# Kernel optimization log

Hardware: AMD Instinct MI355X
Metric: run time of the kernel (lower is better)

## Reference

```python
import jax, jax.numpy as jnp
import numpy as np

MARGIN = 0.5  # hardcoded in the torch __init__ regardless of the margin arg
P_IDS, K_PER_ID, K_PER_MOD = 32, 8, 4
B, C = P_IDS * K_PER_ID, 1024


def setup_inputs() -> dict:
    key = jax.random.key(0)
    inputs = jax.random.normal(key, (B, C), dtype=jnp.float32)
    # Standard cross-modal ReID sampler: P identities, K instances each,
    # first K/2 from modality 0, last K/2 from modality 1. This guarantees the
    # boolean-mask reshape in the original code is well-formed (M per row).
    targets = jnp.repeat(jnp.arange(P_IDS, dtype=jnp.int32), K_PER_ID)
    subs = jnp.tile(jnp.repeat(jnp.arange(2, dtype=jnp.int32), K_PER_MOD), P_IDS)
    return {"inputs": inputs, "targets": targets, "subs": subs, "m_count": K_PER_MOD}


def _loss(inputs, targets, subs, m_count):
    b, c = inputs.shape
    # Mask construction uses detached inputs in the original (clone().detach()).
    xs = jax.lax.stop_gradient(inputs)
    diff = jnp.abs(xs[:, None, :] - xs[None, :, :])                     # (B,B,C)
    identity_mask = targets[:, None] == targets[None, :]                # (B,B)
    modality_mask = subs[:, None] == subs[None, :]                      # (B,B)
    combined = identity_mask & modality_mask                            # (B,B)

    # diff[combined].reshape(B, M, C): every row has exactly m_count trues;
    # stable argsort recovers the selected column indices in ascending order,
    # matching torch's row-major boolean-mask gather.
    order = jnp.argsort(jnp.where(combined, 0, 1), axis=1)              # stable
    idx = order[:, :m_count]                                            # (B,M)
    modality_diff = jnp.take_along_axis(diff, idx[:, :, None], axis=1)  # (B,M,C)

    mean_md = modality_diff.mean(-1, keepdims=True)                     # (B,M,1)
    m_counts = (modality_diff < mean_md * MARGIN).sum(1)                # (B,C) int
    # mdm[i,j,c] = m_counts[i,c] * m_counts[j,c]  (detached float mask)
    mdm = (m_counts[:, None, :] * m_counts[None, :, :]).astype(inputs.dtype)  # (B,B,C)

    mean_d = diff.mean(-1, keepdims=True)                               # (B,B,1)
    idm = (diff < mean_d * MARGIN).astype(inputs.dtype)                 # (B,B,C)

    # Gradient-carrying pairwise differences (vectorized form of the B-loop).
    d = inputs[:, None, :] - inputs[None, :, :]                         # (B,B,C)
    mod_dist = jnp.sqrt(jnp.maximum(((d * mdm) ** 2).sum(-1), 1e-12))   # (B,B)
    id_dist = jnp.sqrt(jnp.maximum(((d * idm) ** 2).sum(-1), 1e-12))    # (B,B)
    id_dist = jnp.where(identity_mask, jnp.inf, id_dist)                # drop same-id

    per_row = jnp.maximum(mod_dist.max(axis=1) * 10.0 - id_dist.min(axis=1), 0.0)
    return per_row.mean()


def reference(inputs, targets, subs, m_count):
    return _loss(inputs, targets, subs, m_count)
```

## Files before the change

kernel.cpp:

```cpp
#include <hip/hip_runtime.h>
#include <math.h>

#define BB 256
#define CC 1024
#define CC4 (CC/4)
#define MARGIN 0.5f
#define NTILE 64
#define JPT 4

__global__ __launch_bounds__(64) void mcsq_kernel(
    const float* __restrict__ x, const int* __restrict__ targets,
    const int* __restrict__ subs, const int* __restrict__ m_count_p,
    float* __restrict__ mcsq, float* __restrict__ acc,
    unsigned int* __restrict__ cnt_g)
{
    const int i = blockIdx.x;
    const int lane = threadIdx.x;
    if (i == 0 && lane == 0) { *acc = 0.f; *cnt_g = 0u; }
    const int ti = targets[i], si = subs[i];
    int mc = *m_count_p;
    if (mc > 8) mc = 8;

    unsigned long long masks[4];
    #pragma unroll
    for (int q = 0; q < 4; ++q) {
        const int j = q * 64 + lane;
        masks[q] = __ballot(targets[j] == ti && subs[j] == si);
    }
    int idx[8];
    int cnt = 0;
    for (int q = 0; q < 4 && cnt < mc; ++q) {
        unsigned long long m = masks[q];
        while (m && cnt < mc) {
            const int b = __ffsll(m) - 1;
            idx[cnt++] = q * 64 + b;
            m &= m - 1;
        }
    }
    for (int q = 0; q < 4 && cnt < mc; ++q) {
        unsigned long long m = ~masks[q];
        while (m && cnt < mc) {
            const int b = __ffsll(m) - 1;
            idx[cnt++] = q * 64 + b;
            m &= m - 1;
        }
    }

    const float4* x4 = (const float4*)x;
    float4 xi[4];
    #pragma unroll
    for (int t = 0; t < 4; ++t) xi[t] = x4[(long)i * CC4 + lane + 64 * t];

    float4 c4[4];
    #pragma unroll
    for (int t = 0; t < 4; ++t) c4[t] = make_float4(0.f, 0.f, 0.f, 0.f);

    for (int k = 0; k < cnt; ++k) {
        float4 ad[4];
        float s = 0.f;
        #pragma unroll
        for (int t = 0; t < 4; ++t) {
            const float4 xj = x4[(long)idx[k] * CC4 + lane + 64 * t];
            ad[t].x = fabsf(xi[t].x - xj.x);
            ad[t].y = fabsf(xi[t].y - xj.y);
            ad[t].z = fabsf(xi[t].z - xj.z);
            ad[t].w = fabsf(xi[t].w - xj.w);
            s += ad[t].x + ad[t].y + ad[t].z + ad[t].w;
        }
        #pragma unroll
        for (int off = 32; off > 0; off >>= 1) s += __shfl_xor(s, off, 64);
        const float thr = s * (MARGIN / CC);
        #pragma unroll
        for (int t = 0; t < 4; ++t) {
            c4[t].x += (ad[t].x < thr) ? 1.f : 0.f;
            c4[t].y += (ad[t].y < thr) ? 1.f : 0.f;
            c4[t].z += (ad[t].z < thr) ? 1.f : 0.f;
            c4[t].w += (ad[t].w < thr) ? 1.f : 0.f;
        }
    }
    float4* m4 = (float4*)mcsq;
    #pragma unroll
    for (int t = 0; t < 4; ++t) {
        float4 o;
        o.x = c4[t].x * c4[t].x;
        o.y = c4[t].y * c4[t].y;
        o.z = c4[t].z * c4[t].z;
        o.w = c4[t].w * c4[t].w;
        m4[(long)i * CC4 + lane + 64 * t] = o;
    }
}

__global__ __launch_bounds__(256) void pair_kernel(
    const float* __restrict__ x, const float* __restrict__ mcsq,
    const int* __restrict__ targets,
    float* __restrict__ pmax, float* __restrict__ pmin,
    float* __restrict__ pmaxT, float* __restrict__ pminT)
{
    const int tid  = threadIdx.x;
    const int lane = tid & 63;
    const int w    = tid >> 6;
    const int b    = blockIdx.x;

    int jt = (int)((sqrtf(8.0f * (float)b + 1.0f) - 1.0f) * 0.5f);
    if (jt < 0) jt = 0;
    if (jt > 63) jt = 63;
    while (jt > 0 && (jt * (jt + 1)) / 2 > b) --jt;
    while (((jt + 1) * (jt + 2)) / 2 <= b) ++jt;
    const int ig = b - (jt * (jt + 1)) / 2;
    const int i  = ig * 4 + w;
    const int j0 = jt * JPT;

    __shared__ float lds[8192];
    float4* lds4 = (float4*)lds;

    const float4* x4 = (const float4*)x;
    const float4* m4 = (const float4*)mcsq;

    const int ti = targets[i];
    int tj[4];
    #pragma unroll
    for (int q = 0; q < 4; ++q) tj[q] = targets[j0 + q];

    float4 xi[4], mi[4];
    #pragma unroll
    for (int t = 0; t < 4; ++t) {
        const int c4 = lane + 64 * t;
        xi[t] = x4[(long)i * CC4 + c4];
        mi[t] = m4[(long)i * CC4 + c4];
    }

    {
        float4 st[8];
        #pragma unroll
        for (int q = 0; q < 4; ++q) {
            st[q]     = x4[(long)(j0 + q) * CC4 + tid];
            st[4 + q] = m4[(long)(j0 + q) * CC4 + tid];
        }
        #pragma unroll
        for (int q = 0; q < 8; ++q) lds4[q * 256 + tid] = st[q];
    }
    __syncthreads();

    const float4* lx = lds4;
    const float4* lm = lds4 + 1024;

    float mx = 0.f, mn = INFINITY;

    #pragma unroll
    for (int jj = 0; jj < JPT; ++jj) {
        const int j = j0 + jj;

        float4 xa[4];
        float s = 0.f;
        #pragma unroll
        for (int t = 0; t < 4; ++t) {
            xa[t] = lx[jj * 256 + lane + 64 * t];
            s += fabsf(xi[t].x - xa[t].x) + fabsf(xi[t].y - xa[t].y)
               + fabsf(xi[t].z - xa[t].z) + fabsf(xi[t].w - xa[t].w);
        }

        float4 ma[4];
        #pragma unroll
        for (int t = 0; t < 4; ++t) ma[t] = lm[jj * 256 + lane + 64 * t];

        #pragma unroll
        for (int off = 32; off > 0; off >>= 1) s += __shfl_xor(s, off, 64);
        const float thr = s * (MARGIN / CC);

        float ids = 0.f, md = 0.f;
        #pragma unroll
        for (int t = 0; t < 4; ++t) {
            #pragma unroll
            for (int u = 0; u < 4; ++u) {
                const float xiv = (&xi[t].x)[u];
                const float miv = (&mi[t].x)[u];
                const float xav = (&xa[t].x)[u];
                const float mav = (&ma[t].x)[u];
                const float d = xiv - xav;
                const float q = d * d;
                ids += (fabsf(d) < thr) ? q : 0.f;
                md  += q * miv * mav;
            }
        }
        #pragma unroll
        for (int off = 32; off > 0; off >>= 1) {
            ids += __shfl_xor(ids, off, 64);
            md  += __shfl_xor(md,  off, 64);
        }

        const float mod = sqrtf(fmaxf(md, 1e-12f));
        float idv = sqrtf(fmaxf(ids, 1e-12f));
        mx = fmaxf(mx, mod);
        if (tj[jj] != ti) mn = fminf(mn, idv); else idv = INFINITY;

        if (lane == 0) {
            pmaxT[j * BB + i] = mod;
            pminT[j * BB + i] = idv;
        }
    }

    if (lane == 0) {
        pmax[i * NTILE + jt] = mx;
        pmin[i * NTILE + jt] = mn;
    }
}

__global__ __launch_bounds__(64) void final_kernel(
    const float* __restrict__ pmax, const float* __restrict__ pmin,
    const float* __restrict__ pmaxT, const float* __restrict__ pminT,
    float* __restrict__ acc, unsigned int* __restrict__ cnt_g,
    float* __restrict__ out)
{
    const int i = blockIdx.x;
    const int lane = threadIdx.x;
    const int s = i >> 2;
    float mx = 0.f, mn = INFINITY;
    const int t = s + lane;
    if (t < NTILE) {
        mx = fmaxf(mx, pmax[i * NTILE + t]);
        mn = fminf(mn, pmin[i * NTILE + t]);
    }
    const int pv = 4 * s + 4;
    #pragma unroll
    for (int q = 0; q < 4; ++q) {
        const int c = lane + 64 * q;
        if (c < pv) {
            mx = fmaxf(mx, pmaxT[i * BB + c]);
            mn = fminf(mn, pminT[i * BB + c]);
        }
    }
    #pragma unroll
    for (int off = 32; off > 0; off >>= 1) {
        mx = fmaxf(mx, __shfl_xor(mx, off, 64));
        mn = fminf(mn, __shfl_xor(mn, off, 64));
    }
    if (lane == 0) {
        const float per = fmaxf(mx * 10.f - mn, 0.f);
        atomicAdd(acc, per * (1.0f / BB));
        __threadfence();
        const unsigned int old = atomicAdd(cnt_g, 1u);
        if (old == BB - 1) {
            __threadfence();
            out[0] = atomicAdd(acc, 0.0f);
        }
    }
}

extern "C" void kernel_launch(void* const* d_in, const int* in_sizes, int n_in,
                              void* d_out, int out_size, void* d_ws, size_t ws_size,
                              hipStream_t stream)
{
    const float* x       = (const float*)d_in[0];
    const int*   targets = (const int*)d_in[1];
    const int*   subs    = (const int*)d_in[2];
    const int*   m_count = (const int*)d_in[3];
    float* out  = (float*)d_out;

    float* mcsq  = (float*)d_ws;
    float* pmax  = mcsq  + (long)BB * CC;
    float* pmin  = pmax  + BB * NTILE;
    float* pmaxT = pmin  + BB * NTILE;
    float* pminT = pmaxT + BB * BB;
    float* acc   = pminT + BB * BB;
    unsigned int* cnt_g = (unsigned int*)(acc + 1);

    mcsq_kernel <<<BB,   64, 0, stream>>>(x, targets, subs, m_count, mcsq, acc, cnt_g);
    pair_kernel <<<2080, 256, 0, stream>>>(x, mcsq, targets, pmax, pmin, pmaxT, pminT);
    final_kernel<<<BB,   64, 0, stream>>>(pmax, pmin, pmaxT, pminT, acc, cnt_g, out);
}
```

Baseline: 89.04 us.

## Fuse three kernels into one persistent kernel with software grid barriers

Merges the mask-count, pairwise-distance and final-reduction kernels into a single persistent launch of 1024 blocks. The stages are separated by atomic-counter grid barriers, and the 2080 pair tasks are processed in a grid-stride loop. The accumulators are zeroed with a memset beforehand. The aim is to remove kernel launch gaps, at the cost of barrier spin overhead, lower parallelism in the first and last stages, and a deadlock risk if not all 1024 blocks are co-resident.

Result: slower. 268.6 us (+201.6%).

```diff
diff --git a/kernel.cpp b/kernel.cpp
--- a/kernel.cpp
+++ b/kernel.cpp
@@ -7,241 +7,255 @@
 #define MARGIN 0.5f
 #define NTILE 64
 #define JPT 4
-
-__global__ __launch_bounds__(64) void mcsq_kernel(
+#define GRID 1024
+#define NTASK 2080
+
+__device__ __forceinline__ void grid_barrier(unsigned int* ctr,
+                                             unsigned int target, int tid)
+{
+    __syncthreads();
+    if (tid == 0) {
+        __threadfence();
+        atomicAdd(ctr, 1u);
+        while (atomicAdd(ctr, 0u) < target)
+            __builtin_amdgcn_s_sleep(8);
+        __threadfence();
+    }
+    __syncthreads();
+}
+
+__global__ __launch_bounds__(256) void fused_kernel(
     const float* __restrict__ x, const int* __restrict__ targets,
     const int* __restrict__ subs, const int* __restrict__ m_count_p,
-    float* __restrict__ mcsq, float* __restrict__ acc,
-    unsigned int* __restrict__ cnt_g)
-{
-    const int i = blockIdx.x;
-    const int lane = threadIdx.x;
-    if (i == 0 && lane == 0) { *acc = 0.f; *cnt_g = 0u; }
-    const int ti = targets[i], si = subs[i];
-    int mc = *m_count_p;
-    if (mc > 8) mc = 8;
-
-    unsigned long long masks[4];
-    #pragma unroll
-    for (int q = 0; q < 4; ++q) {
-        const int j = q * 64 + lane;
-        masks[q] = __ballot(targets[j] == ti && subs[j] == si);
-    }
-    int idx[8];
-    int cnt = 0;
-    for (int q = 0; q < 4 && cnt < mc; ++q) {
-        unsigned long long m = masks[q];
-        while (m && cnt < mc) {
-            const int b = __ffsll(m) - 1;
-            idx[cnt++] = q * 64 + b;
-            m &= m - 1;
-        }
-    }
-    for (int q = 0; q < 4 && cnt < mc; ++q) {
-        unsigned long long m = ~masks[q];
-        while (m && cnt < mc) {
-            const int b = __ffsll(m) - 1;
-            idx[cnt++] = q * 64 + b;
-            m &= m - 1;
-        }
-    }
-
-    const float4* x4 = (const float4*)x;
-    float4 xi[4];
-    #pragma unroll
-    for (int t = 0; t < 4; ++t) xi[t] = x4[(long)i * CC4 + lane + 64 * t];
-
-    float4 c4[4];
-    #pragma unroll
-    for (int t = 0; t < 4; ++t) c4[t] = make_float4(0.f, 0.f, 0.f, 0.f);
-
-    for (int k = 0; k < cnt; ++k) {
-        float4 ad[4];
-        float s = 0.f;
-        #pragma unroll
-        for (int t = 0; t < 4; ++t) {
-            const float4 xj = x4[(long)idx[k] * CC4 + lane + 64 * t];
-            ad[t].x = fabsf(xi[t].x - xj.x);
-            ad[t].y = fabsf(xi[t].y - xj.y);
-            ad[t].z = fabsf(xi[t].z - xj.z);
-            ad[t].w = fabsf(xi[t].w - xj.w);
-            s += ad[t].x + ad[t].y + ad[t].z + ad[t].w;
-        }
-        #pragma unroll
-        for (int off = 32; off > 0; off >>= 1) s += __shfl_xor(s, off, 64);
-        const float thr = s * (MARGIN / CC);
-        #pragma unroll
-        for (int t = 0; t < 4; ++t) {
-            c4[t].x += (ad[t].x < thr) ? 1.f : 0.f;
-            c4[t].y += (ad[t].y < thr) ? 1.f : 0.f;
-            c4[t].z += (ad[t].z < thr) ? 1.f : 0.f;
-            c4[t].w += (ad[t].w < thr) ? 1.f : 0.f;
-        }
-    }
-    float4* m4 = (float4*)mcsq;
-    #pragma unroll
-    for (int t = 0; t < 4; ++t) {
-        float4 o;
-        o.x = c4[t].x * c4[t].x;
-        o.y = c4[t].y * c4[t].y;
-        o.z = c4[t].z * c4[t].z;
-        o.w = c4[t].w * c4[t].w;
-        m4[(long)i * CC4 + lane + 64 * t] = o;
-    }
-}
-
-__global__ __launch_bounds__(256) void pair_kernel(
-    const float* __restrict__ x, const float* __restrict__ mcsq,
-    const int* __restrict__ targets,
+    float* __restrict__ mcsq,
     float* __restrict__ pmax, float* __restrict__ pmin,
-    float* __restrict__ pmaxT, float* __restrict__ pminT)
+    float* __restrict__ pmaxT, float* __restrict__ pminT,
+    float* __restrict__ acc, unsigned int* __restrict__ cnt_g,
+    unsigned int* __restrict__ bar, float* __restrict__ out)
 {
     const int tid  = threadIdx.x;
     const int lane = tid & 63;
     const int w    = tid >> 6;
-    const int b    = blockIdx.x;
-
-    int jt = (int)((sqrtf(8.0f * (float)b + 1.0f) - 1.0f) * 0.5f);
-    if (jt < 0) jt = 0;
-    if (jt > 63) jt = 63;
-    while (jt > 0 && (jt * (jt + 1)) / 2 > b) --jt;
-    while (((jt + 1) * (jt + 2)) / 2 <= b) ++jt;
-    const int ig = b - (jt * (jt + 1)) / 2;
-    const int i  = ig * 4 + w;
-    const int j0 = jt * JPT;
+    const int bid  = blockIdx.x;
+    const int g    = bid * 4 + w;
 
     __shared__ float lds[8192];
     float4* lds4 = (float4*)lds;
 
     const float4* x4 = (const float4*)x;
+
+    if (g < BB) {
+        const int i = g;
+        const int ti = targets[i], si = subs[i];
+        int mc = *m_count_p;
+        if (mc > 8) mc = 8;
+
+        unsigned long long masks[4];
+        #pragma unroll
+        for (int q = 0; q < 4; ++q) {
+            const int j = q * 64 + lane;
+            masks[q] = __ballot(targets[j] == ti && subs[j] == si);
+        }
+        int idx[8];
+        int cnt = 0;
+        for (int q = 0; q < 4 && cnt < mc; ++q) {
+            unsigned long long m = masks[q];
+            while (m && cnt < mc) {
+                const int b = __ffsll(m) - 1;
+                idx[cnt++] = q * 64 + b;
+                m &= m - 1;
+            }
+        }
+        for (int q = 0; q < 4 && cnt < mc; ++q) {
+            unsigned long long m = ~masks[q];
+            while (m && cnt < mc) {
+                const int b = __ffsll(m) - 1;
+                idx[cnt++] = q * 64 + b;
+                m &= m - 1;
+            }
+        }
+
+        float4 xi[4];
+        #pragma unroll
+        for (int t = 0; t < 4; ++t) xi[t] = x4[(long)i * CC4 + lane + 64 * t];
+
+        float4 c4[4];
+        #pragma unroll
+        for (int t = 0; t < 4; ++t) c4[t] = make_float4(0.f, 0.f, 0.f, 0.f);
+
+        for (int k = 0; k < cnt; ++k) {
+            float4 ad[4];
+            float s = 0.f;
+            #pragma unroll
+            for (int t = 0; t < 4; ++t) {
+                const float4 xj = x4[(long)idx[k] * CC4 + lane + 64 * t];
+                ad[t].x = fabsf(xi[t].x - xj.x);
+                ad[t].y = fabsf(xi[t].y - xj.y);
+                ad[t].z = fabsf(xi[t].z - xj.z);
+                ad[t].w = fabsf(xi[t].w - xj.w);
+                s += ad[t].x + ad[t].y + ad[t].z + ad[t].w;
+            }
+            #pragma unroll
+            for (int off = 32; off > 0; off >>= 1) s += __shfl_xor(s, off, 64);
+            const float thr = s * (MARGIN / CC);
+            #pragma unroll
+            for (int t = 0; t < 4; ++t) {
+                c4[t].x += (ad[t].x < thr) ? 1.f : 0.f;
+                c4[t].y += (ad[t].y < thr) ? 1.f : 0.f;
+                c4[t].z += (ad[t].z < thr) ? 1.f : 0.f;
+                c4[t].w += (ad[t].w < thr) ? 1.f : 0.f;
+            }
+        }
+        float4* m4o = (float4*)mcsq;
+        #pragma unroll
+        for (int t = 0; t < 4; ++t) {
+            float4 o;
+            o.x = c4[t].x * c4[t].x;
+            o.y = c4[t].y * c4[t].y;
+            o.z = c4[t].z * c4[t].z;
+            o.w = c4[t].w * c4[t].w;
+            m4o[(long)i * CC4 + lane + 64 * t] = o;
+        }
+    }
+
+    grid_barrier(&bar[0], GRID, tid);
+
     const float4* m4 = (const float4*)mcsq;
 
-    const int ti = targets[i];
-    int tj[4];
-    #pragma unroll
-    for (int q = 0; q < 4; ++q) tj[q] = targets[j0 + q];
-
-    float4 xi[4], mi[4];
-    #pragma unroll
-    for (int t = 0; t < 4; ++t) {
-        const int c4 = lane + 64 * t;
-        xi[t] = x4[(long)i * CC4 + c4];
-        mi[t] = m4[(long)i * CC4 + c4];
-    }
-
-    {
-        float4 st[8];
+    for (int T = bid; T < NTASK; T += GRID) {
+        int jt = (int)((sqrtf(8.0f * (float)T + 1.0f) - 1.0f) * 0.5f);
+        if (jt < 0) jt = 0;
+        if (jt > 63) jt = 63;
+        while (jt > 0 && (jt * (jt + 1)) / 2 > T) --jt;
+        while (((jt + 1) * (jt + 2)) / 2 <= T) ++jt;
+        const int ig = T - (jt * (jt + 1)) / 2;
+        const int i  = ig * 4 + w;
+        const int j0 = jt * JPT;
+
+        __syncthreads();
+
+        {
+            float4 st[8];
+            #pragma unroll
+            for (int q = 0; q < 4; ++q) {
+                st[q]     = x4[(long)(j0 + q) * CC4 + tid];
+                st[4 + q] = m4[(long)(j0 + q) * CC4 + tid];
+            }
+            #pragma unroll
+            for (int q = 0; q < 8; ++q) lds4[q * 256 + tid] = st[q];
+        }
+        __syncthreads();
+
+        const int ti = targets[i];
+        int tj[4];
+        #pragma unroll
+        for (int q = 0; q < 4; ++q) tj[q] = targets[j0 + q];
+
+        float4 xi[4], mi[4];
+        #pragma unroll
+        for (int t = 0; t < 4; ++t) {
+            const int c4 = lane + 64 * t;
+            xi[t] = x4[(long)i * CC4 + c4];
+            mi[t] = m4[(long)i * CC4 + c4];
+        }
+
+        const float4* lx = lds4;
+        const float4* lm = lds4 + 1024;
+
+        float mx = 0.f, mn = INFINITY;
+
+        #pragma unroll
+        for (int jj = 0; jj < JPT; ++jj) {
+            const int j = j0 + jj;
+
+            float4 xa[4];
+            float s = 0.f;
+            #pragma unroll
+            for (int t = 0; t < 4; ++t) {
+                xa[t] = lx[jj * 256 + lane + 64 * t];
+                s += fabsf(xi[t].x - xa[t].x) + fabsf(xi[t].y - xa[t].y)
+                   + fabsf(xi[t].z - xa[t].z) + fabsf(xi[t].w - xa[t].w);
+            }
+
+            float4 ma[4];
+            #pragma unroll
+            for (int t = 0; t < 4; ++t) ma[t] = lm[jj * 256 + lane + 64 * t];
+
+            #pragma unroll
+            for (int off = 32; off > 0; off >>= 1) s += __shfl_xor(s, off, 64);
+            const float thr = s * (MARGIN / CC);
+
+            float ids = 0.f, md = 0.f;
+            #pragma unroll
+            for (int t = 0; t < 4; ++t) {
+                #pragma unroll
+                for (int u = 0; u < 4; ++u) {
+                    const float xiv = (&xi[t].x)[u];
+                    const float miv = (&mi[t].x)[u];
+                    const float xav = (&xa[t].x)[u];
+                    const float mav = (&ma[t].x)[u];
+                    const float d = xiv - xav;
+                    const float q = d * d;
+                    ids += (fabsf(d) < thr) ? q : 0.f;
+                    md  += q * miv * mav;
+                }
+            }
+            #pragma unroll
+            for (int off = 32; off > 0; off >>= 1) {
+                ids += __shfl_xor(ids, off, 64);
+                md  += __shfl_xor(md,  off, 64);
+            }
+
+            const float mod = sqrtf(fmaxf(md, 1e-12f));
+            float idv = sqrtf(fmaxf(ids, 1e-12f));
+            mx = fmaxf(mx, mod);
+            if (tj[jj] != ti) mn = fminf(mn, idv); else idv = INFINITY;
+
+            if (lane == 0) {
+                pmaxT[j * BB + i] = mod;
+                pminT[j * BB + i] = idv;
+            }
+        }
+        if (lane == 0) {
+            pmax[i * NTILE + jt] = mx;
+            pmin[i * NTILE + jt] = mn;
+        }
+    }
+
+    grid_barrier(&bar[1], GRID, tid);
+
+    if (g < BB) {
+        const int i = g;
+        const int s = i >> 2;
+        float mx = 0.f, mn = INFINITY;
+        const int t = s + lane;
+        if (t < NTILE) {
+            mx = fmaxf(mx, pmax[i * NTILE + t]);
+            mn = fminf(mn, pmin[i * NTILE + t]);
+        }
+        const int pv = 4 * s + 4;
         #pragma unroll
         for (int q = 0; q < 4; ++q) {
-            st[q]     = x4[(long)(j0 + q) * CC4 + tid];
-            st[4 + q] = m4[(long)(j0 + q) * CC4 + tid];
-        }
-        #pragma unroll
-        for (int q = 0; q < 8; ++q) lds4[q * 256 + tid] = st[q];
-    }
-    __syncthreads();
-
-    const float4* lx = lds4;
-    const float4* lm = lds4 + 1024;
-
-    float mx = 0.f, mn = INFINITY;
-
-    #pragma unroll
-    for (int jj = 0; jj < JPT; ++jj) {
-        const int j = j0 + jj;
-
-        float4 xa[4];
-        float s = 0.f;
-        #pragma unroll
-        for (int t = 0; t < 4; ++t) {
-            xa[t] = lx[jj * 256 + lane + 64 * t];
-            s += fabsf(xi[t].x - xa[t].x) + fabsf(xi[t].y - xa[t].y)
-               + fabsf(xi[t].z - xa[t].z) + fabsf(xi[t].w - xa[t].w);
-        }
-
-        float4 ma[4];
-        #pragma unroll
-        for (int t = 0; t < 4; ++t) ma[t] = lm[jj * 256 + lane + 64 * t];
-
-        #pragma unroll
-        for (int off = 32; off > 0; off >>= 1) s += __shfl_xor(s, off, 64);
-        const float thr = s * (MARGIN / CC);
-
-        float ids = 0.f, md = 0.f;
-        #pragma unroll
-        for (int t = 0; t < 4; ++t) {
-            #pragma unroll
-            for (int u = 0; u < 4; ++u) {
-                const float xiv = (&xi[t].x)[u];
-                const float miv = (&mi[t].x)[u];
-                const float xav = (&xa[t].x)[u];
-                const float mav = (&ma[t].x)[u];
-                const float d = xiv - xav;
-                const float q = d * d;
-                ids += (fabsf(d) < thr) ? q : 0.f;
-                md  += q * miv * mav;
+            const int c = lane + 64 * q;
+            if (c < pv) {
+                mx = fmaxf(mx, pmaxT[i * BB + c]);
+                mn = fminf(mn, pminT[i * BB + c]);
             }
         }
         #pragma unroll
         for (int off = 32; off > 0; off >>= 1) {
-            ids += __shfl_xor(ids, off, 64);
-            md  += __shfl_xor(md,  off, 64);
-        }
-
-        const float mod = sqrtf(fmaxf(md, 1e-12f));
-        float idv = sqrtf(fmaxf(ids, 1e-12f));
-        mx = fmaxf(mx, mod);
-        if (tj[jj] != ti) mn = fminf(mn, idv); else idv = INFINITY;
-
+            mx = fmaxf(mx, __shfl_xor(mx, off, 64));
+            mn = fminf(mn, __shfl_xor(mn, off, 64));
+        }
         if (lane == 0) {
-            pmaxT[j * BB + i] = mod;
-            pminT[j * BB + i] = idv;
-        }
-    }
-
-    if (lane == 0) {
-        pmax[i * NTILE + jt] = mx;
-        pmin[i * NTILE + jt] = mn;
-    }
-}
-
-__global__ __launch_bounds__(64) void final_kernel(
-    const float* __restrict__ pmax, const float* __restrict__ pmin,
-    const float* __restrict__ pmaxT, const float* __restrict__ pminT,
-    float* __restrict__ acc, unsigned int* __restrict__ cnt_g,
-    float* __restrict__ out)
-{
-    const int i = blockIdx.x;
-    const int lane = threadIdx.x;
-    const int s = i >> 2;
-    float mx = 0.f, mn = INFINITY;
-    const int t = s + lane;
-    if (t < NTILE) {
-        mx = fmaxf(mx, pmax[i * NTILE + t]);
-        mn = fminf(mn, pmin[i * NTILE + t]);
-    }
-    const int pv = 4 * s + 4;
-    #pragma unroll
-    for (int q = 0; q < 4; ++q) {
-        const int c = lane + 64 * q;
-        if (c < pv) {
-            mx = fmaxf(mx, pmaxT[i * BB + c]);
-            mn = fminf(mn, pminT[i * BB + c]);
-        }
-    }
-    #pragma unroll
-    for (int off = 32; off > 0; off >>= 1) {
-        mx = fmaxf(mx, __shfl_xor(mx, off, 64));
-        mn = fminf(mn, __shfl_xor(mn, off, 64));
-    }
-    if (lane == 0) {
-        const float per = fmaxf(mx * 10.f - mn, 0.f);
-        atomicAdd(acc, per * (1.0f / BB));
-        __threadfence();
-        const unsigned int old = atomicAdd(cnt_g, 1u);
-        if (old == BB - 1) {
+            const float per = fmaxf(mx * 10.f - mn, 0.f);
+            atomicAdd(acc, per * (1.0f / BB));
             __threadfence();
-            out[0] = atomicAdd(acc, 0.0f);
+            const unsigned int old = atomicAdd(cnt_g, 1u);
+            if (old == BB - 1) {
+                __threadfence();
+                out[0] = atomicAdd(acc, 0.0f);
+            }
         }
     }
 }
@@ -263,8 +277,11 @@
     float* pminT = pmaxT + BB * BB;
     float* acc   = pminT + BB * BB;
     unsigned int* cnt_g = (unsigned int*)(acc + 1);
-
-    mcsq_kernel <<<BB,   64, 0, stream>>>(x, targets, subs, m_count, mcsq, acc, cnt_g);
-    pair_kernel <<<2080, 256, 0, stream>>>(x, mcsq, targets, pmax, pmin, pmaxT, pminT);
-    final_kernel<<<BB,   64, 0, stream>>>(pmax, pmin, pmaxT, pminT, acc, cnt_g, out);
+    unsigned int* bar   = cnt_g + 1;
+
+    hipMemsetAsync(acc, 0, 16, stream);
+
+    fused_kernel<<<GRID, 256, 0, stream>>>(
+        x, targets, subs, m_count, mcsq, pmax, pmin, pmaxT, pminT,
+        acc, cnt_g, bar, out);
 }
```
